# Performance work log

Measured on AMD Instinct MI355X. Metric: run time of the kernel, lower is better.

Reference implementation:

```python
import jax, jax.numpy as jnp
import numpy as np

# ---- module config (from init_kwargs) ----
VOL_RANGE = np.array([-40.0, -40.0, -4.0, 40.0, 40.0, 4.0], np.float32)
VOXEL_SIZE = 0.4
GRID = tuple(int(v) for v in ((VOL_RANGE[3:] - VOL_RANGE[:3]) / VOXEL_SIZE).astype(np.int32))  # (200,200,20)
SIGMA_FACTOR = 3.0
OPACITY_THRESH = 1e-4
EPS = 1e-6
K = 8  # fixed local window per Gaussian (covers 3*sigma_max/voxel_size span)

B, N, C = 1, 25000, 8


def setup_inputs() -> dict:
    key = jax.random.key(0)
    k1, k2, k3, k4, k5 = jax.random.split(key, 5)
    lo = jnp.asarray(VOL_RANGE[:3]) + 1.0
    hi = jnp.asarray(VOL_RANGE[3:]) - 1.0
    means3d = lo + (hi - lo) * jax.random.uniform(k1, (B, N, 3), jnp.float32)
    opacities = jax.random.uniform(k2, (B, N, 1), jnp.float32)
    scales = 0.05 + 0.3 * jax.random.uniform(k3, (B, N, 3), jnp.float32)  # sigma_max=0.35m -> <=6 voxel span
    rotations = jax.random.normal(k4, (B, N, 4), jnp.float32)
    features = jax.random.normal(k5, (B, N, C), jnp.float32)
    return {"means3d": means3d, "opacities": opacities, "scales": scales,
            "rotations": rotations, "features": features}


def quat_scale_to_cov(scales, rotations):
    # matches CUDAVoxelizer._get_covariance
    q = rotations / jnp.sqrt(jnp.sum(rotations ** 2, -1, keepdims=True) + 1e-8)
    r, x, y, z = q[..., 0], q[..., 1], q[..., 2], q[..., 3]
    R = jnp.stack([
        1 - 2 * (y * y + z * z), 2 * (x * y - r * z), 2 * (x * z + r * y),
        2 * (x * y + r * z), 1 - 2 * (x * x + z * z), 2 * (y * z - r * x),
        2 * (x * z - r * y), 2 * (y * z + r * x), 1 - 2 * (x * x + y * y),
    ], axis=-1).reshape(q.shape[:-1] + (3, 3))
    L = R * scales[..., None, :]  # R @ diag(scales)
    return L @ jnp.swapaxes(L, -1, -2)


def voxelize_one(means, opac, cov, feats):
    """means [N,3], opac [N,1], cov [N,3,3], feats [N,C] -> density [X,Y,Z,1], gfeat [X,Y,Z,C]."""
    X, Y, Z = GRID
    V = X * Y * Z
    vol_min = jnp.asarray(VOL_RANGE[:3])
    vol_max = jnp.asarray(VOL_RANGE[3:])
    gmax = jnp.asarray(GRID, jnp.int32) - 1

    sigma = jnp.sqrt(jnp.diagonal(cov, axis1=-2, axis2=-1))          # [N,3]
    bmin = means - SIGMA_FACTOR * sigma
    bmax = means + SIGMA_FACTOR * sigma
    # _filter_gaussians_torch as a multiplicative mask (removed Gaussians contribute 0)
    keep = (jnp.all(bmax > vol_min, -1) & jnp.all(bmin < vol_max, -1)
            & (opac[:, 0] > OPACITY_THRESH))                          # [N]

    cov_inv = jnp.linalg.inv(cov)                                     # [N,3,3]
    bmin_s = jax.lax.stop_gradient(bmin)
    bmax_s = jax.lax.stop_gradient(bmax)
    # torch .int() truncates toward zero; clamp as in fallback
    idx_min = jnp.maximum(((bmin_s - vol_min) / VOXEL_SIZE).astype(jnp.int32), 0)     # [N,3]
    idx_max = jnp.minimum(((bmax_s - vol_min) / VOXEL_SIZE).astype(jnp.int32), gmax)  # [N,3]

    o = jnp.arange(K, dtype=jnp.int32)
    offs = jnp.stack(jnp.meshgrid(o, o, o, indexing='ij'), -1).reshape(-1, 3)  # [P,3], P=K^3
    vox = idx_min[:, None, :] + offs[None]                            # [N,P,3]
    valid = jnp.all(vox <= idx_max[:, None, :], -1)                   # [N,P]

    centers = vox.astype(jnp.float32) * VOXEL_SIZE + vol_min + 0.5 * VOXEL_SIZE
    diff = centers - means[:, None, :]                                # [N,P,3]
    maha = jnp.einsum('npi,nij,npj->np', diff, cov_inv, diff)
    contrib = opac * jnp.exp(-0.5 * maha)                             # [N,P] (opac [N,1] bcast)
    contrib = jnp.where(valid & keep[:, None], contrib, 0.0)

    flat = (vox[..., 0] * Y + vox[..., 1]) * Z + vox[..., 2]
    flat = jnp.clip(flat, 0, V - 1).reshape(-1)                       # zeroed contribs land harmlessly

    density = jnp.zeros((V,), jnp.float32).at[flat].add(contrib.reshape(-1))
    gfeat = jnp.zeros((V, C), jnp.float32).at[flat].add(
        (contrib[..., None] * feats[:, None, :]).reshape(-1, C))
    gfeat = gfeat / jnp.clip(density, EPS)[:, None]
    return density.reshape(X, Y, Z, 1), gfeat.reshape(X, Y, Z, C)


def reference(means3d, opacities, scales, rotations, features):
    cov = quat_scale_to_cov(scales.reshape(-1, 3), rotations.reshape(-1, 4))
    cov = cov.reshape(means3d.shape[0], -1, 3, 3)
    density, gfeat = jax.vmap(voxelize_one)(means3d, opacities, cov, features)
    return density, gfeat
```

## Files before the change

### kernel.cpp

```cpp
#include <hip/hip_runtime.h>

namespace {
constexpr int GX = 200, GY = 200, GZ = 20;
constexpr int NVOX = GX * GY * GZ;
constexpr float VMINX = -40.f, VMINY = -40.f, VMINZ = -4.f;
constexpr float VMAXX =  40.f, VMAXY =  40.f, VMAXZ =  4.f;
constexpr float VS    = 0.4f;
constexpr float HVS   = 0.2f;
constexpr float SIGF  = 3.0f;

constexpr int TILE   = 4;
constexpr int ZSEG   = 4;
constexpr int TX     = GX / TILE;
constexpr int TY     = GY / TILE;
constexpr int TZ     = GZ / ZSEG;
constexpr int NTILES = TX * TY * TZ;
constexpr int CAP    = 128;
constexpr int PSTRIDE = 20;
}

__device__ __forceinline__ bool gauss_setup(
    const float* __restrict__ means, const float* __restrict__ opacs,
    const float* __restrict__ scales, const float* __restrict__ rots,
    int g,
    int& gx0, int& gx1, int& gy0, int& gy1, int& gz0, int& gz1,
    float& c0, float& c1, float& c2, float& c3, float& c4, float& c5,
    float& mx, float& my, float& mz, float& lop)
{
    const float op = opacs[g];
    mx = means[3*g+0]; my = means[3*g+1]; mz = means[3*g+2];
    const float sx = scales[3*g+0], sy = scales[3*g+1], sz = scales[3*g+2];
    const float q0 = rots[4*g+0], q1 = rots[4*g+1], q2 = rots[4*g+2], q3 = rots[4*g+3];

    const float qn = sqrtf(q0*q0 + q1*q1 + q2*q2 + q3*q3 + 1e-8f);
    const float r = q0/qn, x = q1/qn, y = q2/qn, z = q3/qn;

    const float R00 = 1.f - 2.f*(y*y + z*z), R01 = 2.f*(x*y - r*z), R02 = 2.f*(x*z + r*y);
    const float R10 = 2.f*(x*y + r*z), R11 = 1.f - 2.f*(x*x + z*z), R12 = 2.f*(y*z - r*x);
    const float R20 = 2.f*(x*z - r*y), R21 = 2.f*(y*z + r*x), R22 = 1.f - 2.f*(x*x + y*y);

    const float s0 = sx*sx, s1 = sy*sy, s2 = sz*sz;
    const float v00 = R00*R00*s0 + R01*R01*s1 + R02*R02*s2;
    const float v01 = R00*R10*s0 + R01*R11*s1 + R02*R12*s2;
    const float v02 = R00*R20*s0 + R01*R21*s1 + R02*R22*s2;
    const float v11 = R10*R10*s0 + R11*R11*s1 + R12*R12*s2;
    const float v12 = R10*R20*s0 + R11*R21*s1 + R12*R22*s2;
    const float v22 = R20*R20*s0 + R21*R21*s1 + R22*R22*s2;

    const float sgx = SIGF * sqrtf(v00), sgy = SIGF * sqrtf(v11), sgz = SIGF * sqrtf(v22);
    const float bminx = mx - sgx, bminy = my - sgy, bminz = mz - sgz;
    const float bmaxx = mx + sgx, bmaxy = my + sgy, bmaxz = mz + sgz;

    const bool keep = (bmaxx > VMINX) && (bmaxy > VMINY) && (bmaxz > VMINZ)
                   && (bminx < VMAXX) && (bminy < VMAXY) && (bminz < VMAXZ)
                   && (op > 1e-4f);
    if (!keep) return false;

    gx0 = max((int)((bminx - VMINX) / VS), 0);
    gy0 = max((int)((bminy - VMINY) / VS), 0);
    gz0 = max((int)((bminz - VMINZ) / VS), 0);
    gx1 = min((int)((bmaxx - VMINX) / VS), GX - 1);
    gy1 = min((int)((bmaxy - VMINY) / VS), GY - 1);
    gz1 = min((int)((bmaxz - VMINZ) / VS), GZ - 1);
    gx1 = min(gx1, gx0 + 7);
    gy1 = min(gy1, gy0 + 7);
    gz1 = min(gz1, gz0 + 7);
    if (gx1 < gx0 || gy1 < gy0 || gz1 < gz0) return false;

    const float m00 = v11*v22 - v12*v12;
    const float m01 = v02*v12 - v01*v22;
    const float m02 = v01*v12 - v02*v11;
    const float det = v00*m00 + v01*m01 + v02*m02;
    const float id  = 1.f / det;
    const float i00 = m00*id, i01 = m01*id, i02 = m02*id;
    const float i11 = (v00*v22 - v02*v02)*id;
    const float i12 = (v01*v02 - v00*v12)*id;
    const float i22 = (v00*v11 - v01*v01)*id;

    c0 = -0.5f * i00; c3 = -0.5f * i11; c5 = -0.5f * i22;
    c1 = -i01; c2 = -i02; c4 = -i12;
    lop = logf(op);
    return true;
}

__global__ __launch_bounds__(64) void voxel_bin(
    const float* __restrict__ means, const float* __restrict__ opacs,
    const float* __restrict__ scales, const float* __restrict__ rots,
    const float* __restrict__ feats,
    int* __restrict__ counts, int* __restrict__ entries,
    float* __restrict__ params, int N)
{
    const int g = blockIdx.x * blockDim.x + threadIdx.x;
    if (g >= N) return;
    int gx0, gx1, gy0, gy1, gz0, gz1;
    float c0,c1,c2,c3,c4,c5, mx,my,mz, lop;
    if (!gauss_setup(means, opacs, scales, rots, g,
                     gx0,gx1,gy0,gy1,gz0,gz1, c0,c1,c2,c3,c4,c5, mx,my,mz, lop))
        return;

    float* P = params + (size_t)g * PSTRIDE;
    *(float4*)(P + 0)  = make_float4(c0, c1, c2, c3);
    *(float4*)(P + 4)  = make_float4(c4, c5, mx, my);
    *(float4*)(P + 8)  = make_float4(mz, lop,
                                     __int_as_float(gx0 | (gy0<<8) | (gz0<<16)),
                                     __int_as_float(gx1 | (gy1<<8) | (gz1<<16)));
    *(float4*)(P + 12) = *(const float4*)(feats + 8*g);
    *(float4*)(P + 16) = *(const float4*)(feats + 8*g + 4);

    const int tx0 = gx0 >> 2, tx1 = gx1 >> 2;
    const int ty0 = gy0 >> 2, ty1 = gy1 >> 2;
    const int tz0 = gz0 >> 2, tz1 = gz1 >> 2;
    for (int tx = tx0; tx <= tx1; ++tx)
        for (int ty = ty0; ty <= ty1; ++ty)
            for (int tz = tz0; tz <= tz1; ++tz) {
                const int t = (tx * TY + ty) * TZ + tz;
                const int slot = atomicAdd(&counts[t], 1);
                if (slot < CAP) entries[t * CAP + slot] = g;
            }
}

__global__ __launch_bounds__(64) void voxel_gather(
    const float* __restrict__ params,
    const int* __restrict__ counts, const int* __restrict__ entries,
    float* __restrict__ density, float* __restrict__ gfeat)
{
    __shared__ float gs[CAP][PSTRIDE];

    const int tile = blockIdx.x;
    const int seg  = tile % TZ;
    const int txy  = tile / TZ;
    const int ttx  = txy / TY, tty = txy % TY;
    const int tid  = threadIdx.x;
    const int cnt  = min(counts[tile], CAP);

    for (int j = tid; j < cnt; j += 64) {
        const int g = entries[tile * CAP + j];
        const float* P = params + (size_t)g * PSTRIDE;
        float4* G = (float4*)gs[j];
        G[0] = *(const float4*)(P + 0);
        G[1] = *(const float4*)(P + 4);
        G[2] = *(const float4*)(P + 8);
        G[3] = *(const float4*)(P + 12);
        G[4] = *(const float4*)(P + 16);
    }
    __syncthreads();

    const int lz = tid & 3, ly = (tid >> 2) & 3, lx = tid >> 4;
    const int vx = ttx * TILE + lx, vy = tty * TILE + ly, vz = seg * ZSEG + lz;
    const float cx = (float)vx * VS + VMINX + HVS;
    const float cy = (float)vy * VS + VMINY + HVS;
    const float cz = (float)vz * VS + VMINZ + HVS;

    float den = 0.f;
    float ft0 = 0.f, ft1 = 0.f, ft2 = 0.f, ft3 = 0.f;
    float ft4 = 0.f, ft5 = 0.f, ft6 = 0.f, ft7 = 0.f;

    #pragma unroll 2
    for (int j = 0; j < cnt; ++j) {
        const float4* G = (const float4*)gs[j];
        const float4 p0 = G[0];
        const float4 p1 = G[1];
        const float4 p2 = G[2];
        const float4 p3 = G[3];
        const float4 p4 = G[4];

        const int w0 = __float_as_int(p2.z);
        const int w1 = __float_as_int(p2.w);
        const int gx0 = w0 & 255, gy0 = (w0 >> 8) & 255, gz0 = (w0 >> 16) & 255;
        const int gx1 = w1 & 255, gy1 = (w1 >> 8) & 255, gz1 = (w1 >> 16) & 255;
        const bool inw = (vx >= gx0) & (vx <= gx1) & (vy >= gy0) & (vy <= gy1)
                       & (vz >= gz0) & (vz <= gz1);

        const float ddx = cx - p1.z, ddy = cy - p1.w, ddz = cz - p2.x;
        const float ex = p2.y + ddx*(p0.x*ddx + p0.y*ddy + p0.z*ddz)
                              + ddy*(p0.w*ddy + p1.x*ddz) + p1.y*ddz*ddz;
        float w = __expf(ex);
        w = inw ? w : 0.f;
        den += w;
        ft0 += w * p3.x; ft1 += w * p3.y; ft2 += w * p3.z; ft3 += w * p3.w;
        ft4 += w * p4.x; ft5 += w * p4.y; ft6 += w * p4.z; ft7 += w * p4.w;
    }

    const int flat = (vx * GY + vy) * GZ + vz;
    density[flat] = den;
    const float inv = 1.f / fmaxf(den, 1e-6f);
    float4 oa = make_float4(ft0*inv, ft1*inv, ft2*inv, ft3*inv);
    float4 ob = make_float4(ft4*inv, ft5*inv, ft6*inv, ft7*inv);
    *(float4*)(gfeat + (size_t)flat * 8)     = oa;
    *(float4*)(gfeat + (size_t)flat * 8 + 4) = ob;
}

extern "C" void kernel_launch(void* const* d_in, const int* in_sizes, int n_in,
                              void* d_out, int out_size, void* d_ws, size_t ws_size,
                              hipStream_t stream)
{
    const float* means  = (const float*)d_in[0];
    const float* opacs  = (const float*)d_in[1];
    const float* scales = (const float*)d_in[2];
    const float* rots   = (const float*)d_in[3];
    const float* feats  = (const float*)d_in[4];

    float* density = (float*)d_out;
    float* gfeat   = density + NVOX;
    const int N = in_sizes[0] / 3;

    int*   counts  = (int*)d_ws;
    int*   entries = counts + NTILES;
    float* params  = (float*)(entries + (size_t)NTILES * CAP);

    hipMemsetAsync(counts, 0, NTILES * sizeof(int), stream);

    voxel_bin<<<(N + 63) / 64, 64, 0, stream>>>(means, opacs, scales, rots, feats,
                                                counts, entries, params, N);
    voxel_gather<<<NTILES, 64, 0, stream>>>(params, counts, entries, density, gfeat);
}
```

Measured before the change: 103.8 us.

## Pack Gaussian params to fp16/bf16 and process two z voxels per thread

Gaussian parameters are compressed to 48 bytes each: fp16 conic coefficients, bf16 features, and a bit-packed window holding start plus extent. Each thread now accumulates two voxels four apart in z, sharing the xy part of the quadratic form. Tiles become 4x4x8, which halves the number of tiles and roughly halves the binning atomics and duplicate shared-memory loads. The cost is lower precision in the coefficients and features, which may break tolerance, plus more registers per thread and extra work in the partial last z tile.

```diff
diff --git a/kernel.cpp b/kernel.cpp
--- a/kernel.cpp
+++ b/kernel.cpp
@@ -1,4 +1,5 @@
 #include <hip/hip_runtime.h>
+#include <hip/hip_fp16.h>
 
 namespace {
 constexpr int GX = 200, GY = 200, GZ = 20;
@@ -10,13 +11,18 @@
 constexpr float SIGF  = 3.0f;
 
 constexpr int TILE   = 4;
-constexpr int ZSEG   = 4;
+constexpr int ZSEG   = 8;
 constexpr int TX     = GX / TILE;
 constexpr int TY     = GY / TILE;
-constexpr int TZ     = GZ / ZSEG;
+constexpr int TZ     = (GZ + ZSEG - 1) / ZSEG;
 constexpr int NTILES = TX * TY * TZ;
 constexpr int CAP    = 128;
-constexpr int PSTRIDE = 20;
+constexpr int PSTRIDE = 12;
+}
+
+__device__ __forceinline__ unsigned bf_rne(float f) {
+    unsigned u = __float_as_uint(f);
+    return (u + 0x7fffu + ((u >> 16) & 1u)) >> 16;
 }
 
 __device__ __forceinline__ bool gauss_setup(
@@ -98,18 +104,34 @@
                      gx0,gx1,gy0,gy1,gz0,gz1, c0,c1,c2,c3,c4,c5, mx,my,mz, lop))
         return;
 
+    const unsigned cc01 = (unsigned)__half_as_ushort(__float2half(c0))
+                        | ((unsigned)__half_as_ushort(__float2half(c1)) << 16);
+    const unsigned cc23 = (unsigned)__half_as_ushort(__float2half(c2))
+                        | ((unsigned)__half_as_ushort(__float2half(c3)) << 16);
+    const unsigned cc45 = (unsigned)__half_as_ushort(__float2half(c4))
+                        | ((unsigned)__half_as_ushort(__float2half(c5)) << 16);
+    const unsigned win  = (unsigned)gx0 | ((unsigned)gy0 << 8) | ((unsigned)gz0 << 16)
+                        | ((unsigned)(gx1 - gx0) << 21)
+                        | ((unsigned)(gy1 - gy0) << 24)
+                        | ((unsigned)(gz1 - gz0) << 27);
+
+    const float4 f0 = *(const float4*)(feats + 8*g);
+    const float4 f1 = *(const float4*)(feats + 8*g + 4);
+    const unsigned fb01 = bf_rne(f0.x) | (bf_rne(f0.y) << 16);
+    const unsigned fb23 = bf_rne(f0.z) | (bf_rne(f0.w) << 16);
+    const unsigned fb45 = bf_rne(f1.x) | (bf_rne(f1.y) << 16);
+    const unsigned fb67 = bf_rne(f1.z) | (bf_rne(f1.w) << 16);
+
     float* P = params + (size_t)g * PSTRIDE;
-    *(float4*)(P + 0)  = make_float4(c0, c1, c2, c3);
-    *(float4*)(P + 4)  = make_float4(c4, c5, mx, my);
-    *(float4*)(P + 8)  = make_float4(mz, lop,
-                                     __int_as_float(gx0 | (gy0<<8) | (gz0<<16)),
-                                     __int_as_float(gx1 | (gy1<<8) | (gz1<<16)));
-    *(float4*)(P + 12) = *(const float4*)(feats + 8*g);
-    *(float4*)(P + 16) = *(const float4*)(feats + 8*g + 4);
+    *(float4*)(P + 0) = make_float4(__uint_as_float(cc01), __uint_as_float(cc23),
+                                    __uint_as_float(cc45), __uint_as_float(win));
+    *(float4*)(P + 4) = make_float4(mx, my, mz, lop);
+    *(float4*)(P + 8) = make_float4(__uint_as_float(fb01), __uint_as_float(fb23),
+                                    __uint_as_float(fb45), __uint_as_float(fb67));
 
     const int tx0 = gx0 >> 2, tx1 = gx1 >> 2;
     const int ty0 = gy0 >> 2, ty1 = gy1 >> 2;
-    const int tz0 = gz0 >> 2, tz1 = gz1 >> 2;
+    const int tz0 = gz0 >> 3, tz1 = gz1 >> 3;
     for (int tx = tx0; tx <= tx1; ++tx)
         for (int ty = ty0; ty <= ty1; ++ty)
             for (int tz = tz0; tz <= tz1; ++tz) {
@@ -127,7 +149,7 @@
     __shared__ float gs[CAP][PSTRIDE];
 
     const int tile = blockIdx.x;
-    const int seg  = tile % TZ;
+    const int tz   = tile % TZ;
     const int txy  = tile / TZ;
     const int ttx  = txy / TY, tty = txy % TY;
     const int tid  = threadIdx.x;
@@ -140,54 +162,84 @@
         G[0] = *(const float4*)(P + 0);
         G[1] = *(const float4*)(P + 4);
         G[2] = *(const float4*)(P + 8);
-        G[3] = *(const float4*)(P + 12);
-        G[4] = *(const float4*)(P + 16);
     }
     __syncthreads();
 
     const int lz = tid & 3, ly = (tid >> 2) & 3, lx = tid >> 4;
-    const int vx = ttx * TILE + lx, vy = tty * TILE + ly, vz = seg * ZSEG + lz;
-    const float cx = (float)vx * VS + VMINX + HVS;
-    const float cy = (float)vy * VS + VMINY + HVS;
-    const float cz = (float)vz * VS + VMINZ + HVS;
-
-    float den = 0.f;
-    float ft0 = 0.f, ft1 = 0.f, ft2 = 0.f, ft3 = 0.f;
-    float ft4 = 0.f, ft5 = 0.f, ft6 = 0.f, ft7 = 0.f;
+    const int vx = ttx * TILE + lx, vy = tty * TILE + ly;
+    const int vz1 = tz * ZSEG + lz;
+    const int vz2 = vz1 + 4;
+    const float cx  = (float)vx * VS + VMINX + HVS;
+    const float cy  = (float)vy * VS + VMINY + HVS;
+    const float cz1 = (float)vz1 * VS + VMINZ + HVS;
+
+    float den1 = 0.f, den2 = 0.f;
+    float fa0=0.f,fa1=0.f,fa2=0.f,fa3=0.f,fa4=0.f,fa5=0.f,fa6=0.f,fa7=0.f;
+    float fb0=0.f,fb1=0.f,fb2=0.f,fb3=0.f,fb4=0.f,fb5=0.f,fb6=0.f,fb7=0.f;
 
     #pragma unroll 2
     for (int j = 0; j < cnt; ++j) {
         const float4* G = (const float4*)gs[j];
-        const float4 p0 = G[0];
-        const float4 p1 = G[1];
-        const float4 p2 = G[2];
-        const float4 p3 = G[3];
-        const float4 p4 = G[4];
-
-        const int w0 = __float_as_int(p2.z);
-        const int w1 = __float_as_int(p2.w);
-        const int gx0 = w0 & 255, gy0 = (w0 >> 8) & 255, gz0 = (w0 >> 16) & 255;
-        const int gx1 = w1 & 255, gy1 = (w1 >> 8) & 255, gz1 = (w1 >> 16) & 255;
-        const bool inw = (vx >= gx0) & (vx <= gx1) & (vy >= gy0) & (vy <= gy1)
-                       & (vz >= gz0) & (vz <= gz1);
-
-        const float ddx = cx - p1.z, ddy = cy - p1.w, ddz = cz - p2.x;
-        const float ex = p2.y + ddx*(p0.x*ddx + p0.y*ddy + p0.z*ddz)
-                              + ddy*(p0.w*ddy + p1.x*ddz) + p1.y*ddz*ddz;
-        float w = __expf(ex);
-        w = inw ? w : 0.f;
-        den += w;
-        ft0 += w * p3.x; ft1 += w * p3.y; ft2 += w * p3.z; ft3 += w * p3.w;
-        ft4 += w * p4.x; ft5 += w * p4.y; ft6 += w * p4.z; ft7 += w * p4.w;
+        const float4 q0 = G[0];
+        const float4 q1 = G[1];
+        const float4 q2 = G[2];
+
+        const unsigned u01 = __float_as_uint(q0.x);
+        const unsigned u23 = __float_as_uint(q0.y);
+        const unsigned u45 = __float_as_uint(q0.z);
+        const float c0 = __half2float(__ushort_as_half((unsigned short)(u01 & 0xffffu)));
+        const float c1 = __half2float(__ushort_as_half((unsigned short)(u01 >> 16)));
+        const float c2 = __half2float(__ushort_as_half((unsigned short)(u23 & 0xffffu)));
+        const float c3 = __half2float(__ushort_as_half((unsigned short)(u23 >> 16)));
+        const float c4 = __half2float(__ushort_as_half((unsigned short)(u45 & 0xffffu)));
+        const float c5 = __half2float(__ushort_as_half((unsigned short)(u45 >> 16)));
+
+        const unsigned w = __float_as_uint(q0.w);
+        const int gx0 = (int)(w & 255u),        gx1 = gx0 + (int)((w >> 21) & 7u);
+        const int gy0 = (int)((w >> 8) & 255u), gy1 = gy0 + (int)((w >> 24) & 7u);
+        const int gz0 = (int)((w >> 16) & 31u), gz1 = gz0 + (int)((w >> 27) & 7u);
+        const bool inxy = (vx >= gx0) & (vx <= gx1) & (vy >= gy0) & (vy <= gy1);
+        const bool in1  = inxy & (vz1 >= gz0) & (vz1 <= gz1);
+        const bool in2  = inxy & (vz2 >= gz0) & (vz2 <= gz1);
+
+        const float ddx = cx - q1.x, ddy = cy - q1.y;
+        const float axy = q1.w + ddx*(c0*ddx + c1*ddy) + c3*ddy*ddy;
+        const float czs = c2*ddx + c4*ddy;
+        const float dz1 = cz1 - q1.z;
+        const float dz2 = dz1 + 4.f * VS;
+        float w1 = __expf(axy + dz1*(czs + c5*dz1));
+        float w2 = __expf(axy + dz2*(czs + c5*dz2));
+        w1 = in1 ? w1 : 0.f;
+        w2 = in2 ? w2 : 0.f;
+
+        const unsigned b01 = __float_as_uint(q2.x), b23 = __float_as_uint(q2.y);
+        const unsigned b45 = __float_as_uint(q2.z), b67 = __float_as_uint(q2.w);
+        const float f0 = __uint_as_float(b01 << 16), f1 = __uint_as_float(b01 & 0xffff0000u);
+        const float f2 = __uint_as_float(b23 << 16), f3 = __uint_as_float(b23 & 0xffff0000u);
+        const float f4 = __uint_as_float(b45 << 16), f5 = __uint_as_float(b45 & 0xffff0000u);
+        const float f6 = __uint_as_float(b67 << 16), f7 = __uint_as_float(b67 & 0xffff0000u);
+
+        den1 += w1;
+        fa0 += w1*f0; fa1 += w1*f1; fa2 += w1*f2; fa3 += w1*f3;
+        fa4 += w1*f4; fa5 += w1*f5; fa6 += w1*f6; fa7 += w1*f7;
+        den2 += w2;
+        fb0 += w2*f0; fb1 += w2*f1; fb2 += w2*f2; fb3 += w2*f3;
+        fb4 += w2*f4; fb5 += w2*f5; fb6 += w2*f6; fb7 += w2*f7;
     }
 
-    const int flat = (vx * GY + vy) * GZ + vz;
-    density[flat] = den;
-    const float inv = 1.f / fmaxf(den, 1e-6f);
-    float4 oa = make_float4(ft0*inv, ft1*inv, ft2*inv, ft3*inv);
-    float4 ob = make_float4(ft4*inv, ft5*inv, ft6*inv, ft7*inv);
-    *(float4*)(gfeat + (size_t)flat * 8)     = oa;
-    *(float4*)(gfeat + (size_t)flat * 8 + 4) = ob;
+    const int flat1 = (vx * GY + vy) * GZ + vz1;
+    density[flat1] = den1;
+    const float inv1 = 1.f / fmaxf(den1, 1e-6f);
+    *(float4*)(gfeat + (size_t)flat1 * 8)     = make_float4(fa0*inv1, fa1*inv1, fa2*inv1, fa3*inv1);
+    *(float4*)(gfeat + (size_t)flat1 * 8 + 4) = make_float4(fa4*inv1, fa5*inv1, fa6*inv1, fa7*inv1);
+
+    if (vz2 < GZ) {
+        const int flat2 = flat1 + 4;
+        density[flat2] = den2;
+        const float inv2 = 1.f / fmaxf(den2, 1e-6f);
+        *(float4*)(gfeat + (size_t)flat2 * 8)     = make_float4(fb0*inv2, fb1*inv2, fb2*inv2, fb3*inv2);
+        *(float4*)(gfeat + (size_t)flat2 * 8 + 4) = make_float4(fb4*inv2, fb5*inv2, fb6*inv2, fb7*inv2);
+    }
 }
 
 extern "C" void kernel_launch(void* const* d_in, const int* in_sizes, int n_in,
@@ -205,7 +257,7 @@
     const int N = in_sizes[0] / 3;
 
     int*   counts  = (int*)d_ws;
-    int*   entries = counts + NTILES;
+    int*   entries = counts + ((NTILES + 63) & ~63);
     float* params  = (float*)(entries + (size_t)NTILES * CAP);
 
     hipMemsetAsync(counts, 0, NTILES * sizeof(int), stream);
```

New measurement: 102.6 us. Within noise of the previous version (-1.1%).
